# Performance work log

Hardware: AMD Instinct MI355X
Metric: run time of the kernel (lower is better)

## Reference

```python
import jax, jax.numpy as jnp
import numpy as np

HIDDEN = 1024
NUM_HEAD = 16
HEAD_DIM = HIDDEN // NUM_HEAD
B, S = 2, 2048


def setup_inputs() -> dict:
    key = jax.random.key(0)
    ks = jax.random.split(key, 9)
    scale = 1.0 / np.sqrt(HIDDEN)
    X = jax.random.normal(ks[0], (B, S, HIDDEN), dtype=jnp.float32)
    # causal mask, broadcastable over heads: [B, 1, S, S]
    causal = jnp.tril(jnp.ones((S, S), dtype=jnp.int32))
    mask = jnp.broadcast_to(causal[None, None, :, :], (B, 1, S, S))
    Wq = jax.random.normal(ks[1], (HIDDEN, HIDDEN), dtype=jnp.float32) * scale
    bq = jnp.zeros((HIDDEN,), dtype=jnp.float32)
    Wk = jax.random.normal(ks[2], (HIDDEN, HIDDEN), dtype=jnp.float32) * scale
    bk = jnp.zeros((HIDDEN,), dtype=jnp.float32)
    Wv = jax.random.normal(ks[3], (HIDDEN, HIDDEN), dtype=jnp.float32) * scale
    bv = jnp.zeros((HIDDEN,), dtype=jnp.float32)
    Wo = jax.random.normal(ks[4], (HIDDEN, HIDDEN), dtype=jnp.float32) * scale
    bo = jnp.zeros((HIDDEN,), dtype=jnp.float32)
    return {"X": X, "mask": mask, "Wq": Wq, "bq": bq, "Wk": Wk, "bk": bk,
            "Wv": Wv, "bv": bv, "Wo": Wo, "bo": bo}


def reference(X, mask, Wq, bq, Wk, bk, Wv, bv, Wo, bo):
    bsz, seq_len, _ = X.shape
    # Q/K/V projections (torch Linear: x @ W.T + b; here W stored as [in, out])
    Q = X @ Wq + bq
    K = X @ Wk + bk
    V = X @ Wv + bv
    # [B, H, S, D]
    Q = Q.reshape(bsz, seq_len, NUM_HEAD, HEAD_DIM).transpose(0, 2, 1, 3)
    K = K.reshape(bsz, seq_len, NUM_HEAD, HEAD_DIM).transpose(0, 2, 1, 3)
    V = V.reshape(bsz, seq_len, NUM_HEAD, HEAD_DIM).transpose(0, 2, 1, 3)
    # scores: [B, H, S, S]
    scores = jnp.einsum('bhqd,bhkd->bhqk', Q, K) / jnp.sqrt(
        jnp.asarray(HEAD_DIM, dtype=X.dtype))
    scores = jnp.where(mask == 0, jnp.asarray(-jnp.inf, dtype=scores.dtype), scores)
    # dropout (rate=0.0) is identity; softmax over keys
    attn = jax.nn.softmax(scores, axis=-1)
    out = jnp.einsum('bhqk,bhkd->bhqd', attn, V)
    out = out.transpose(0, 2, 1, 3).reshape(bsz, seq_len, HIDDEN)
    return out @ Wo + bo
```

## Files before the change

### kernel.cpp

```cpp
#include <hip/hip_runtime.h>
#include <stdint.h>

#define HID 1024
#define SEQ 2048
#define NB 2
#define NH 16
#define HD 64
#define MROWS 4096

typedef float f32x4 __attribute__((ext_vector_type(4)));
typedef short s16x4 __attribute__((ext_vector_type(4)));
typedef short s16x8 __attribute__((ext_vector_type(8)));
typedef uint32_t u32x4 __attribute__((ext_vector_type(4)));

#define MFMA16(a, b, c) __builtin_amdgcn_mfma_f32_16x16x32_bf16((a), (b), (c), 0, 0, 0)

#define GLOAD_LDS16(gp, lp)                                                    \
  __builtin_amdgcn_global_load_lds(                                            \
      (const __attribute__((address_space(1))) unsigned int*)(gp),             \
      (__attribute__((address_space(3))) unsigned int*)(lp), 16, 0, 0)

__device__ __forceinline__ short f2bf(float x) {
  uint32_t u = __builtin_bit_cast(uint32_t, x);
  u += 0x7fffu + ((u >> 16) & 1u);
  return (short)(u >> 16);
}

__device__ __forceinline__ uint32_t cvtpk(float lo, float hi) {
  uint32_t r;
  asm("v_cvt_pk_bf16_f32 %0, %1, %2" : "=v"(r) : "v"(lo), "v"(hi));
  return r;
}

__global__ __launch_bounds__(256) void prep_kernel(
    const float* __restrict__ X, const float* __restrict__ w0,
    const float* __restrict__ w1, const float* __restrict__ w2,
    const float* __restrict__ w3, short* __restrict__ Xb,
    short* __restrict__ Wtall) {
  const int z = blockIdx.z;
  if (z == 4) {
    const size_t i = ((size_t)blockIdx.y * 32 + blockIdx.x) * 256 + threadIdx.x;
    const float* s = X + i * 16;
    short* d = Xb + i * 16;
#pragma unroll
    for (int h = 0; h < 2; h++) {
      f32x4 a = *(const f32x4*)(s + h * 8);
      f32x4 b = *(const f32x4*)(s + h * 8 + 4);
      s16x8 o;
      o[0] = f2bf(a[0]); o[1] = f2bf(a[1]); o[2] = f2bf(a[2]); o[3] = f2bf(a[3]);
      o[4] = f2bf(b[0]); o[5] = f2bf(b[1]); o[6] = f2bf(b[2]); o[7] = f2bf(b[3]);
      *(s16x8*)(d + h * 8) = o;
    }
    return;
  }
  __shared__ float t[32][33];
  const float* src = (z == 0) ? w0 : (z == 1) ? w1 : (z == 2) ? w2 : w3;
  short* dst = Wtall + ((size_t)z << 20);
  const int tx = threadIdx.x & 31, ty = threadIdx.x >> 5;
  const int r0 = blockIdx.y * 32, c0 = blockIdx.x * 32;
#pragma unroll
  for (int i = 0; i < 4; i++)
    t[ty + i * 8][tx] = src[(size_t)(r0 + ty + i * 8) * HID + c0 + tx];
  __syncthreads();
#pragma unroll
  for (int i = 0; i < 4; i++)
    dst[(size_t)(c0 + ty + i * 8) * HID + r0 + tx] = f2bf(t[tx][ty + i * 8]);
}

template <int EPI, int MI>
__global__ __launch_bounds__(256) void gemm_bf16(
    const short* __restrict__ A, const short* __restrict__ Bt,
    const float* __restrict__ b0, const float* __restrict__ b1,
    const float* __restrict__ b2, short* __restrict__ Qb, short* __restrict__ Kg,
    short* __restrict__ Vg, float* __restrict__ Out) {
  __shared__ char lds[2][MI * 2048 + 8192];
  const int tid = threadIdx.x;
  const int w = tid >> 6, l = tid & 63, lg = l >> 4, ln = l & 15;
  const int wm = w >> 1, wn = w & 1;
  const int m0 = blockIdx.y * (32 * MI), n0 = blockIdx.x * 128;

  f32x4 acc[MI][4];
#pragma unroll
  for (int i = 0; i < MI; i++)
#pragma unroll
    for (int j = 0; j < 4; j++) acc[i][j] = f32x4{0.f, 0.f, 0.f, 0.f};

  auto stage = [&](int buf, int k0) {
#pragma unroll
    for (int i = 0; i < MI / 2; i++) {
      const int c = i * 256 + tid;
      const int row = c >> 2;
      const int cs = (c & 3) ^ (row & 3);
      GLOAD_LDS16(A + (size_t)(m0 + row) * 1024 + k0 + cs * 8,
                  lds[buf] + c * 16);
    }
#pragma unroll
    for (int i = 0; i < 2; i++) {
      const int c = i * 256 + tid;
      const int row = c >> 2;
      const int cs = (c & 3) ^ (row & 3);
      GLOAD_LDS16(Bt + (size_t)(n0 + row) * 1024 + k0 + cs * 8,
                  lds[buf] + MI * 2048 + c * 16);
    }
  };

  stage(0, 0);
  for (int kt = 0; kt < 32; ++kt) {
    const int cur = kt & 1;
    if (kt < 31) {
      stage(cur ^ 1, (kt + 1) * 32);
      if constexpr (MI == 4)
        asm volatile("s_waitcnt vmcnt(4)" ::: "memory");
      else
        asm volatile("s_waitcnt vmcnt(3)" ::: "memory");
    } else {
      asm volatile("s_waitcnt vmcnt(0)" ::: "memory");
    }
    __builtin_amdgcn_s_barrier();
    __builtin_amdgcn_sched_barrier(0);

    const char* ldsc = lds[cur];
    s16x8 af[MI], bfr[4];
#pragma unroll
    for (int mi = 0; mi < MI; mi++) {
      const int row = wm * (16 * MI) + mi * 16 + ln;
      af[mi] = *(const s16x8*)(ldsc + row * 64 + ((lg ^ (row & 3)) * 16));
    }
#pragma unroll
    for (int ni = 0; ni < 4; ni++) {
      const int row = wn * 64 + ni * 16 + ln;
      bfr[ni] =
          *(const s16x8*)(ldsc + MI * 2048 + row * 64 + ((lg ^ (row & 3)) * 16));
    }
#pragma unroll
    for (int mi = 0; mi < MI; mi++)
#pragma unroll
      for (int ni = 0; ni < 4; ni++)
        acc[mi][ni] = MFMA16(af[mi], bfr[ni], acc[mi][ni]);

    __builtin_amdgcn_s_barrier();
    __builtin_amdgcn_sched_barrier(0);
  }

  const float QSC = 0.18033688011112042f;
#pragma unroll
  for (int ni = 0; ni < 4; ni++) {
    const int c = n0 + wn * 64 + ni * 16 + ln;
    if (EPI == 0) {
      const int mat = c >> 10, cc = c & 1023, hh = cc >> 6, d = cc & 63;
      const float* bp = (mat == 0) ? b0 : (mat == 1) ? b1 : b2;
      const float bias = bp[cc];
#pragma unroll
      for (int mi = 0; mi < MI; mi++) {
#pragma unroll
        for (int r = 0; r < 4; r++) {
          const int m = m0 + wm * (16 * MI) + mi * 16 + lg * 4 + r;
          const int bb = m >> 11, s = m & 2047;
          const float fv = acc[mi][ni][r] + bias;
          const size_t bh = (size_t)(bb * 16 + hh);
          if (mat == 0) {
            Qb[(bh * SEQ + s) * HD + d] = f2bf(fv * QSC);
          } else if (mat == 1) {
            const int tile = s >> 6, rr = s & 63;
            Kg[bh * (SEQ * HD) + tile * 4096 + rr * 64 +
               ((((d >> 3) ^ (rr & 7)) << 3) | (d & 7))] = f2bf(fv);
          } else {
            const int sp = (s & ~31) | ((s & 12) << 1) | (((s >> 4) & 1) << 2) |
                           (s & 3);
            const int tile = sp >> 6, kp = sp & 63;
            Vg[bh * (SEQ * HD) + tile * 4096 + d * 64 +
               ((((kp >> 3) ^ (d & 7)) << 3) | (kp & 7))] = f2bf(fv);
          }
        }
      }
    } else {
      const float bias = b0[c];
#pragma unroll
      for (int mi = 0; mi < MI; mi++)
#pragma unroll
        for (int r = 0; r < 4; r++) {
          const int m = m0 + wm * (16 * MI) + mi * 16 + lg * 4 + r;
          Out[(size_t)m * 1024 + c] = acc[mi][ni][r] + bias;
        }
    }
  }
}


__device__ __forceinline__ void stage_tile(const short* Kt, const short* Vt,
                                           int t, char* buf, int w, int l) {
  const char* src = (w < 2) ? ((const char*)(Kt + (size_t)t * 4096) + (w & 1) * 4096)
                            : ((const char*)(Vt + (size_t)t * 4096) + (w & 1) * 4096);
  char* dst = buf + ((w < 2) ? 0 : 8192) + (w & 1) * 4096;
#pragma unroll
  for (int j = 0; j < 4; j++)
    GLOAD_LDS16(src + j * 1024 + l * 16, dst + j * 1024);
}

template <bool MASK>
__device__ __forceinline__ void softmax_pv(f32x4 st[4], const s16x8 vf[2][4],
                                           const s16x8& ones, f32x4 o[4],
                                           float& m2, float& l_run, int k0,
                                           int qrow, int lg) {
  float p[4][4];
#pragma unroll
  for (int mt = 0; mt < 4; mt++)
#pragma unroll
    for (int r = 0; r < 4; r++) {
      float v = st[mt][r];
      if (MASK) {
        const int key = k0 + mt * 16 + lg * 4 + r;
        if (key > qrow) v = -3e38f;
      }
      p[mt][r] = v;
    }
  float a0 = fmaxf(fmaxf(p[0][0], p[0][1]), fmaxf(p[0][2], p[0][3]));
  float a1 = fmaxf(fmaxf(p[1][0], p[1][1]), fmaxf(p[1][2], p[1][3]));
  float a2 = fmaxf(fmaxf(p[2][0], p[2][1]), fmaxf(p[2][2], p[2][3]));
  float a3 = fmaxf(fmaxf(p[3][0], p[3][1]), fmaxf(p[3][2], p[3][3]));
  float pmax = fmaxf(fmaxf(a0, a1), fmaxf(a2, a3));

  if (!__all(pmax <= m2 + 8.0f)) {
    pmax = fmaxf(pmax, __shfl_xor(pmax, 16));
    pmax = fmaxf(pmax, __shfl_xor(pmax, 32));
    const float m_new = fmaxf(m2, pmax);
    const float corr = exp2f(m2 - m_new);
    l_run *= corr;
#pragma unroll
    for (int i = 0; i < 4; i++) o[i] *= corr;
    m2 = m_new;
  }
#pragma unroll
  for (int mt = 0; mt < 4; mt++)
#pragma unroll
    for (int r = 0; r < 4; r++) p[mt][r] = exp2f(p[mt][r] - m2);

  s16x8 pf[2];
#pragma unroll
  for (int s = 0; s < 2; s++) {
    u32x4 wv;
    wv[0] = cvtpk(p[s * 2][0], p[s * 2][1]);
    wv[1] = cvtpk(p[s * 2][2], p[s * 2][3]);
    wv[2] = cvtpk(p[s * 2 + 1][0], p[s * 2 + 1][1]);
    wv[3] = cvtpk(p[s * 2 + 1][2], p[s * 2 + 1][3]);
    pf[s] = __builtin_bit_cast(s16x8, wv);
  }
  f32x4 ps = f32x4{0.f, 0.f, 0.f, 0.f};
  ps = MFMA16(ones, pf[0], ps);
  ps = MFMA16(ones, pf[1], ps);
#pragma unroll
  for (int s = 0; s < 2; s++)
#pragma unroll
    for (int vmt = 0; vmt < 4; vmt++)
      o[vmt] = MFMA16(vf[s][vmt], pf[s], o[vmt]);
  l_run += ps[0];
}

template <bool MASK>
__device__ __forceinline__ void compute_tile(const char* cbuf, const s16x8& qf0,
                                             const s16x8& qf1, const s16x8& ones,
                                             int k0, int qrow, int lg, int ln,
                                             float& m2, float& l_run, f32x4 o[4]) {
  const int x = ln & 7;
  f32x4 st[4];
#pragma unroll
  for (int mt = 0; mt < 4; mt++) {
    const char* rowp = cbuf + (mt * 16 + ln) * 128;
    const s16x8 k0f = *(const s16x8*)(rowp + ((lg ^ x) * 16));
    const s16x8 k1f = *(const s16x8*)(rowp + (((4 + lg) ^ x) * 16));
    st[mt] = f32x4{0.f, 0.f, 0.f, 0.f};
    st[mt] = MFMA16(k0f, qf0, st[mt]);
    st[mt] = MFMA16(k1f, qf1, st[mt]);
  }
  s16x8 vf[2][4];
#pragma unroll
  for (int s = 0; s < 2; s++)
#pragma unroll
    for (int vmt = 0; vmt < 4; vmt++)
      vf[s][vmt] = *(const s16x8*)(cbuf + 8192 + (vmt * 16 + ln) * 128 +
                                   (((s * 4 + lg) ^ x) * 16));
  softmax_pv<MASK>(st, vf, ones, o, m2, l_run, k0, qrow, lg);
}

__device__ __forceinline__ void attn_group_pass(const short* Kt, const short* Vt,
                                                const short* __restrict__ Qb,
                                                short* __restrict__ Ob, int bh,
                                                int G, int w, int l, char* lds) {
  const int lg = l >> 4, ln = l & 15;
  const int qrow = G * 64 + w * 16 + ln;
  const short* Qp = Qb + ((size_t)bh * SEQ + qrow) * HD;
  const s16x8 qf0 = *(const s16x8*)(Qp + lg * 8);
  const s16x8 qf1 = *(const s16x8*)(Qp + 32 + lg * 8);
  s16x8 ones;
#pragma unroll
  for (int j = 0; j < 8; j++) ones[j] = (short)0x3F80;

  float m2 = -3e38f, l_run = 0.f;
  f32x4 o[4];
#pragma unroll
  for (int i = 0; i < 4; i++) o[i] = f32x4{0.f, 0.f, 0.f, 0.f};

  const int nt = G + 1;
  stage_tile(Kt, Vt, 0, lds, w, l);
  for (int t = 0; t < nt - 1; ++t) {
    stage_tile(Kt, Vt, t + 1, lds + ((t + 1) & 1) * 16384, w, l);
    asm volatile("s_waitcnt vmcnt(4)" ::: "memory");
    __builtin_amdgcn_s_barrier();
    __builtin_amdgcn_sched_barrier(0);
    compute_tile<false>(lds + (t & 1) * 16384, qf0, qf1, ones, t * 64, qrow, lg,
                        ln, m2, l_run, o);
    __builtin_amdgcn_s_barrier();
    __builtin_amdgcn_sched_barrier(0);
  }
  asm volatile("s_waitcnt vmcnt(0)" ::: "memory");
  __builtin_amdgcn_s_barrier();
  __builtin_amdgcn_sched_barrier(0);
  compute_tile<true>(lds + ((nt - 1) & 1) * 16384, qf0, qf1, ones, (nt - 1) * 64,
                     qrow, lg, ln, m2, l_run, o);
  __builtin_amdgcn_s_barrier();
  __builtin_amdgcn_sched_barrier(0);

  const float inv = 1.0f / l_run;
  const int bb = bh >> 4, hh = bh & 15;
  const size_t orow = (size_t)(bb * SEQ + qrow) * HID + hh * HD;
#pragma unroll
  for (int mt = 0; mt < 4; mt++) {
    s16x4 ov;
#pragma unroll
    for (int r = 0; r < 4; r++) ov[r] = f2bf(o[mt][r] * inv);
    *(s16x4*)(Ob + orow + mt * 16 + lg * 4) = ov;
  }
}

__global__ __launch_bounds__(256) void attn_kernel(const short* __restrict__ Qb,
                                                   const short* __restrict__ Kg,
                                                   const short* __restrict__ Vg,
                                                   short* __restrict__ Ob) {
  __shared__ char lds[32768];
  const int bid = blockIdx.x;
  const int L = (bid & 7) * 64 + (bid >> 3);
  const int bh = L >> 4, g = L & 15;
  const int w = threadIdx.x >> 6, l = threadIdx.x & 63;
  const short* Kt = Kg + (size_t)bh * (SEQ * HD);
  const short* Vt = Vg + (size_t)bh * (SEQ * HD);
  attn_group_pass(Kt, Vt, Qb, Ob, bh, g, w, l, lds);
  attn_group_pass(Kt, Vt, Qb, Ob, bh, 31 - g, w, l, lds);
}

extern "C" void kernel_launch(void* const* d_in, const int* in_sizes, int n_in,
                              void* d_out, int out_size, void* d_ws,
                              size_t ws_size, hipStream_t stream) {
  const float* X = (const float*)d_in[0];
  const float* Wq = (const float*)d_in[2];
  const float* bq = (const float*)d_in[3];
  const float* Wk = (const float*)d_in[4];
  const float* bk = (const float*)d_in[5];
  const float* Wv = (const float*)d_in[6];
  const float* bv = (const float*)d_in[7];
  const float* Wo = (const float*)d_in[8];
  const float* bo = (const float*)d_in[9];
  float* out = (float*)d_out;

  char* ws = (char*)d_ws;
  short* Xb = (short*)(ws);
  short* Wtall = (short*)(ws + (8u << 20));
  short* Qb = (short*)(ws + (16u << 20));
  short* Kg = (short*)(ws + (24u << 20));
  short* Vg = (short*)(ws + (32u << 20));
  short* Ob = (short*)(ws + (40u << 20));
  short* Wto = Wtall + (3u << 20);

  prep_kernel<<<dim3(32, 32, 5), 256, 0, stream>>>(X, Wq, Wk, Wv, Wo, Xb, Wtall);

  gemm_bf16<0, 4><<<dim3(24, 32), 256, 0, stream>>>(Xb, Wtall, bq, bk, bv, Qb,
                                                    Kg, Vg, nullptr);
  attn_kernel<<<512, 256, 0, stream>>>(Qb, Kg, Vg, Ob);
  gemm_bf16<1, 2><<<dim3(8, 64), 256, 0, stream>>>(Ob, Wto, bo, nullptr, nullptr,
                                                   nullptr, nullptr, nullptr,
                                                   out);
}
```

Before: 212.6 us.

## Triple-buffer attention K/V LDS tiles and drop per-tile trailing barrier

New measurement: 219.5 us. 1.03x slower.

```diff
diff --git a/kernel.cpp b/kernel.cpp
--- a/kernel.cpp
+++ b/kernel.cpp
@@ -188,37 +188,55 @@
 
 
 __device__ __forceinline__ void stage_tile(const short* Kt, const short* Vt,
-                                           int t, char* buf, int w, int l) {
+                                           int t, char* sdst, int bufoff, int w) {
   const char* src = (w < 2) ? ((const char*)(Kt + (size_t)t * 4096) + (w & 1) * 4096)
                             : ((const char*)(Vt + (size_t)t * 4096) + (w & 1) * 4096);
-  char* dst = buf + ((w < 2) ? 0 : 8192) + (w & 1) * 4096;
+  char* dst = sdst + bufoff;
 #pragma unroll
   for (int j = 0; j < 4; j++)
-    GLOAD_LDS16(src + j * 1024 + l * 16, dst + j * 1024);
-}
-
-template <bool MASK>
-__device__ __forceinline__ void softmax_pv(f32x4 st[4], const s16x8 vf[2][4],
-                                           const s16x8& ones, f32x4 o[4],
-                                           float& m2, float& l_run, int k0,
-                                           int qrow, int lg) {
-  float p[4][4];
-#pragma unroll
-  for (int mt = 0; mt < 4; mt++)
-#pragma unroll
-    for (int r = 0; r < 4; r++) {
-      float v = st[mt][r];
-      if (MASK) {
+    GLOAD_LDS16(src + j * 1024 + ((threadIdx.x & 63) * 16), dst + j * 1024);
+}
+
+template <int BUF, bool MASK>
+__device__ __forceinline__ void compute_tile(const char* pA, const char* pB,
+                                             const s16x8& qf0, const s16x8& qf1,
+                                             const s16x8& ones, int k0, int qrow,
+                                             int lg, float& m2, float& l_run,
+                                             f32x4 o[4]) {
+  f32x4 st[4];
+  __builtin_amdgcn_s_setprio(1);
+#pragma unroll
+  for (int mt = 0; mt < 4; mt++) {
+    const s16x8 k0f = *(const s16x8*)(pA + BUF + mt * 2048);
+    const s16x8 k1f = *(const s16x8*)(pB + BUF + mt * 2048);
+    st[mt] = f32x4{0.f, 0.f, 0.f, 0.f};
+    st[mt] = MFMA16(k0f, qf0, st[mt]);
+    st[mt] = MFMA16(k1f, qf1, st[mt]);
+  }
+  __builtin_amdgcn_s_setprio(0);
+  s16x8 vf[2][4];
+#pragma unroll
+  for (int vmt = 0; vmt < 4; vmt++) {
+    vf[0][vmt] = *(const s16x8*)(pA + BUF + 8192 + vmt * 2048);
+    vf[1][vmt] = *(const s16x8*)(pB + BUF + 8192 + vmt * 2048);
+  }
+  if (MASK) {
+#pragma unroll
+    for (int mt = 0; mt < 4; mt++)
+#pragma unroll
+      for (int r = 0; r < 4; r++) {
         const int key = k0 + mt * 16 + lg * 4 + r;
-        if (key > qrow) v = -3e38f;
+        if (key > qrow) st[mt][r] = -3e38f;
       }
-      p[mt][r] = v;
-    }
-  float a0 = fmaxf(fmaxf(p[0][0], p[0][1]), fmaxf(p[0][2], p[0][3]));
-  float a1 = fmaxf(fmaxf(p[1][0], p[1][1]), fmaxf(p[1][2], p[1][3]));
-  float a2 = fmaxf(fmaxf(p[2][0], p[2][1]), fmaxf(p[2][2], p[2][3]));
-  float a3 = fmaxf(fmaxf(p[3][0], p[3][1]), fmaxf(p[3][2], p[3][3]));
-  float pmax = fmaxf(fmaxf(a0, a1), fmaxf(a2, a3));
+  }
+  float pmax = fmaxf(fmaxf(st[0][0], st[0][1]), st[0][2]);
+  pmax = fmaxf(fmaxf(pmax, st[0][3]), st[1][0]);
+  pmax = fmaxf(fmaxf(pmax, st[1][1]), st[1][2]);
+  pmax = fmaxf(fmaxf(pmax, st[1][3]), st[2][0]);
+  pmax = fmaxf(fmaxf(pmax, st[2][1]), st[2][2]);
+  pmax = fmaxf(fmaxf(pmax, st[2][3]), st[3][0]);
+  pmax = fmaxf(fmaxf(pmax, st[3][1]), st[3][2]);
+  pmax = fmaxf(pmax, st[3][3]);
 
   if (!__all(pmax <= m2 + 8.0f)) {
     pmax = fmaxf(pmax, __shfl_xor(pmax, 16));
@@ -233,18 +251,19 @@
 #pragma unroll
   for (int mt = 0; mt < 4; mt++)
 #pragma unroll
-    for (int r = 0; r < 4; r++) p[mt][r] = exp2f(p[mt][r] - m2);
+    for (int r = 0; r < 4; r++) st[mt][r] = exp2f(st[mt][r] - m2);
 
   s16x8 pf[2];
 #pragma unroll
   for (int s = 0; s < 2; s++) {
     u32x4 wv;
-    wv[0] = cvtpk(p[s * 2][0], p[s * 2][1]);
-    wv[1] = cvtpk(p[s * 2][2], p[s * 2][3]);
-    wv[2] = cvtpk(p[s * 2 + 1][0], p[s * 2 + 1][1]);
-    wv[3] = cvtpk(p[s * 2 + 1][2], p[s * 2 + 1][3]);
+    wv[0] = cvtpk(st[s * 2][0], st[s * 2][1]);
+    wv[1] = cvtpk(st[s * 2][2], st[s * 2][3]);
+    wv[2] = cvtpk(st[s * 2 + 1][0], st[s * 2 + 1][1]);
+    wv[3] = cvtpk(st[s * 2 + 1][2], st[s * 2 + 1][3]);
     pf[s] = __builtin_bit_cast(s16x8, wv);
   }
+  __builtin_amdgcn_s_setprio(1);
   f32x4 ps = f32x4{0.f, 0.f, 0.f, 0.f};
   ps = MFMA16(ones, pf[0], ps);
   ps = MFMA16(ones, pf[1], ps);
@@ -253,39 +272,19 @@
 #pragma unroll
     for (int vmt = 0; vmt < 4; vmt++)
       o[vmt] = MFMA16(vf[s][vmt], pf[s], o[vmt]);
+  __builtin_amdgcn_s_setprio(0);
   l_run += ps[0];
 }
 
-template <bool MASK>
-__device__ __forceinline__ void compute_tile(const char* cbuf, const s16x8& qf0,
-                                             const s16x8& qf1, const s16x8& ones,
-                                             int k0, int qrow, int lg, int ln,
-                                             float& m2, float& l_run, f32x4 o[4]) {
-  const int x = ln & 7;
-  f32x4 st[4];
-#pragma unroll
-  for (int mt = 0; mt < 4; mt++) {
-    const char* rowp = cbuf + (mt * 16 + ln) * 128;
-    const s16x8 k0f = *(const s16x8*)(rowp + ((lg ^ x) * 16));
-    const s16x8 k1f = *(const s16x8*)(rowp + (((4 + lg) ^ x) * 16));
-    st[mt] = f32x4{0.f, 0.f, 0.f, 0.f};
-    st[mt] = MFMA16(k0f, qf0, st[mt]);
-    st[mt] = MFMA16(k1f, qf1, st[mt]);
-  }
-  s16x8 vf[2][4];
-#pragma unroll
-  for (int s = 0; s < 2; s++)
-#pragma unroll
-    for (int vmt = 0; vmt < 4; vmt++)
-      vf[s][vmt] = *(const s16x8*)(cbuf + 8192 + (vmt * 16 + ln) * 128 +
-                                   (((s * 4 + lg) ^ x) * 16));
-  softmax_pv<MASK>(st, vf, ones, o, m2, l_run, k0, qrow, lg);
-}
+#define CT(BUF, MASKV, K0)                                                     \
+  compute_tile<BUF, MASKV>(pA, pB, qf0, qf1, ones, (K0), qrow, lg, m2, l_run, o)
 
 __device__ __forceinline__ void attn_group_pass(const short* Kt, const short* Vt,
                                                 const short* __restrict__ Qb,
                                                 short* __restrict__ Ob, int bh,
-                                                int G, int w, int l, char* lds) {
+                                                int G, int w, int l, char* lds,
+                                                const char* pA, const char* pB,
+                                                char* sdst) {
   const int lg = l >> 4, ln = l & 15;
   const int qrow = G * 64 + w * 16 + ln;
   const short* Qp = Qb + ((size_t)bh * SEQ + qrow) * HD;
@@ -301,24 +300,27 @@
   for (int i = 0; i < 4; i++) o[i] = f32x4{0.f, 0.f, 0.f, 0.f};
 
   const int nt = G + 1;
-  stage_tile(Kt, Vt, 0, lds, w, l);
+  __builtin_amdgcn_s_barrier();
+  stage_tile(Kt, Vt, 0, sdst, 0, w);
   for (int t = 0; t < nt - 1; ++t) {
-    stage_tile(Kt, Vt, t + 1, lds + ((t + 1) & 1) * 16384, w, l);
+    stage_tile(Kt, Vt, t + 1, sdst, ((t + 1) % 3) * 16384, w);
     asm volatile("s_waitcnt vmcnt(4)" ::: "memory");
     __builtin_amdgcn_s_barrier();
     __builtin_amdgcn_sched_barrier(0);
-    compute_tile<false>(lds + (t & 1) * 16384, qf0, qf1, ones, t * 64, qrow, lg,
-                        ln, m2, l_run, o);
-    __builtin_amdgcn_s_barrier();
-    __builtin_amdgcn_sched_barrier(0);
+    switch (t % 3) {
+      case 0: CT(0, false, t * 64); break;
+      case 1: CT(16384, false, t * 64); break;
+      default: CT(32768, false, t * 64); break;
+    }
   }
   asm volatile("s_waitcnt vmcnt(0)" ::: "memory");
   __builtin_amdgcn_s_barrier();
   __builtin_amdgcn_sched_barrier(0);
-  compute_tile<true>(lds + ((nt - 1) & 1) * 16384, qf0, qf1, ones, (nt - 1) * 64,
-                     qrow, lg, ln, m2, l_run, o);
-  __builtin_amdgcn_s_barrier();
-  __builtin_amdgcn_sched_barrier(0);
+  switch ((nt - 1) % 3) {
+    case 0: CT(0, true, (nt - 1) * 64); break;
+    case 1: CT(16384, true, (nt - 1) * 64); break;
+    default: CT(32768, true, (nt - 1) * 64); break;
+  }
 
   const float inv = 1.0f / l_run;
   const int bb = bh >> 4, hh = bh & 15;
@@ -336,15 +338,19 @@
                                                    const short* __restrict__ Kg,
                                                    const short* __restrict__ Vg,
                                                    short* __restrict__ Ob) {
-  __shared__ char lds[32768];
+  __shared__ char lds[49152];
   const int bid = blockIdx.x;
   const int L = (bid & 7) * 64 + (bid >> 3);
   const int bh = L >> 4, g = L & 15;
   const int w = threadIdx.x >> 6, l = threadIdx.x & 63;
+  const int lg = l >> 4, ln = l & 15, x = ln & 7;
+  const char* pA = lds + ln * 128 + ((lg ^ x) * 16);
+  const char* pB = lds + ln * 128 + (((4 + lg) ^ x) * 16);
+  char* sdst = lds + ((w < 2) ? 0 : 8192) + (w & 1) * 4096 + l * 16;
   const short* Kt = Kg + (size_t)bh * (SEQ * HD);
   const short* Vt = Vg + (size_t)bh * (SEQ * HD);
-  attn_group_pass(Kt, Vt, Qb, Ob, bh, g, w, l, lds);
-  attn_group_pass(Kt, Vt, Qb, Ob, bh, 31 - g, w, l, lds);
+  attn_group_pass(Kt, Vt, Qb, Ob, bh, g, w, l, lds, pA, pB, sdst);
+  attn_group_pass(Kt, Vt, Qb, Ob, bh, 31 - g, w, l, lds, pA, pB, sdst);
 }
 
 extern "C" void kernel_launch(void* const* d_in, const int* in_sizes, int n_in,
```
